# Performance work log

Measured on AMD Instinct MI355X. Metric: run time of the kernel, lower is better.

## Reference

```python
import jax, jax.numpy as jnp
import numpy as np

D_MODEL = 256; N_HEADS = 8; N_LEVELS = 4; N_POINTS = 4
D_HEAD = D_MODEL // N_HEADS


def setup_inputs() -> dict:
    key = jax.random.key(0)
    ks = jax.random.split(key, 8)
    N, Lq = 4, 4096
    shapes = np.array([4096, 2048, 1024, 512], dtype=np.int32)  # temporal lengths per level
    Len_in = int(shapes.sum())  # 7680
    start = np.concatenate([[0], np.cumsum(shapes)[:-1]]).astype(np.int32)
    HLP = N_HEADS * N_LEVELS * N_POINTS
    return {
        "query": jax.random.normal(ks[0], (N, Lq, D_MODEL), jnp.float32),
        "reference_points": jax.random.uniform(ks[1], (N, Lq, N_LEVELS, 1), jnp.float32),
        "input_flatten": jax.random.normal(ks[2], (N, Len_in, D_MODEL), jnp.float32),
        "input_spatial_shapes": jnp.asarray(shapes),
        "input_level_start_index": jnp.asarray(start),
        "W_off": jax.random.normal(ks[3], (D_MODEL, HLP), jnp.float32) * 0.01,
        "b_off": jax.random.normal(ks[4], (HLP,), jnp.float32) * 2.0,
        "W_aw": jax.random.normal(ks[5], (D_MODEL, HLP), jnp.float32) * 0.02,
        "b_aw": jnp.zeros((HLP,), jnp.float32),
        "W_v": jax.random.normal(ks[6], (D_MODEL, D_MODEL), jnp.float32) / np.sqrt(D_MODEL).astype(np.float32),
        "b_v": jnp.zeros((D_MODEL,), jnp.float32),
        "W_out": jax.random.normal(ks[7], (D_MODEL, D_MODEL), jnp.float32) / np.sqrt(D_MODEL).astype(np.float32),
        "b_out": jnp.zeros((D_MODEL,), jnp.float32),
    }


def reference(query, reference_points, input_flatten, input_spatial_shapes,
              input_level_start_index, W_off, b_off, W_aw, b_aw, W_v, b_v,
              W_out, b_out):
    N, Lq, C = query.shape
    M, L, P, Dh = N_HEADS, N_LEVELS, N_POINTS, D_HEAD
    S = input_flatten.shape[1]

    value = (input_flatten @ W_v + b_v).reshape(N, S, M, Dh)
    off = (query @ W_off + b_off).reshape(N, Lq, M, L, P)
    aw = jax.nn.softmax((query @ W_aw + b_aw).reshape(N, Lq, M, L * P), axis=-1)
    aw = aw.reshape(N, Lq, M, L, P)

    # reference_points last dim == 1 branch: loc = ref + off / T_l, in [0,1]
    T = input_spatial_shapes.astype(jnp.float32)[None, None, None, :, None]  # [1,1,1,L,1]
    loc = reference_points[:, :, None, :, None, 0] + off / T  # [N,Lq,M,L,P]

    # grid_sample(align_corners=False, padding_mode='border') along W with H=1, y=0.5:
    # pixel coord x = loc*T - 0.5, clamped to [0, T-1], then linear interp.
    x = jnp.clip(loc * T - 0.5, 0.0, T - 1.0)
    x0 = jnp.floor(x)
    w1 = x - x0                                   # frac weight for right neighbor
    i0 = x0.astype(jnp.int32)
    i1 = jnp.minimum(i0 + 1, input_spatial_shapes[None, None, None, :, None] - 1)
    base = input_level_start_index[None, None, None, :, None]
    g0 = i0 + base                                # global flattened indices [N,Lq,M,L,P]
    g1 = i1 + base

    v = value.transpose(0, 2, 1, 3)               # [N,M,S,Dh]

    def gather(idx):
        idxt = idx.transpose(0, 2, 1, 3, 4).reshape(N, M, Lq * L * P, 1)
        return jnp.take_along_axis(v, idxt, axis=2).reshape(N, M, Lq, L, P, Dh)

    s0 = gather(g0)
    s1 = gather(g1)
    w1t = w1.transpose(0, 2, 1, 3, 4)[..., None]   # [N,M,Lq,L,P,1]
    samp = s0 * (1.0 - w1t) + s1 * w1t             # [N,M,Lq,L,P,Dh]

    awt = aw.transpose(0, 2, 1, 3, 4)[..., None]
    out = (samp * awt).sum(axis=(3, 4))            # [N,M,Lq,Dh]
    out = out.transpose(0, 2, 1, 3).reshape(N, Lq, M * Dh)
    return out @ W_out + b_out
```

## Files before the change

kernel.cpp:

```cpp
#include <hip/hip_runtime.h>
#include <hip/hip_bf16.h>
#include <cstddef>
#include <cstdint>

#define D_MODEL   256
#define N_HEADS   8
#define N_LEVELS  4
#define N_POINTS  4
#define D_HEAD    32
#define HLP       128
#define NBATCH    4
#define LQ        4096
#define S_LEN     7680
#define QB        4

typedef __attribute__((ext_vector_type(8))) short  short8;
typedef __attribute__((ext_vector_type(4))) float  f32x4;
typedef __attribute__((ext_vector_type(8))) unsigned short ushort8;

__device__ __forceinline__ unsigned short f2bf(float x) {
    __hip_bfloat16 h = __float2bfloat16(x);
    return *reinterpret_cast<unsigned short*>(&h);
}
__device__ __forceinline__ float bf2f(unsigned short u) {
    unsigned int v = ((unsigned int)u) << 16;
    return *reinterpret_cast<float*>(&v);
}

__device__ __forceinline__ void gload_lds16(const void* g, void* l) {
    __builtin_amdgcn_global_load_lds(
        (const __attribute__((address_space(1))) void*)g,
        (__attribute__((address_space(3))) void*)l,
        16, 0, 0);
}

__global__ __launch_bounds__(256) void prep_kernel(
    const float* __restrict__ W_v,  const float* __restrict__ W_off,
    const float* __restrict__ W_aw, const float* __restrict__ W_out,
    const float* __restrict__ b_off, const float* __restrict__ b_aw,
    unsigned short* __restrict__ Wv_t, unsigned short* __restrict__ Wcat_t,
    unsigned short* __restrict__ Wout_t, float* __restrict__ bcat)
{
    __shared__ float t[64][65];
    const int z   = blockIdx.z;
    const int k0  = blockIdx.y * 64;
    const int n0  = blockIdx.x * 64;
    const int tid = threadIdx.x;

    const float* src; int srcN; int cs; unsigned short* dst;
    if (z == 0)      { src = W_v;   srcN = 256; cs = n0;       dst = Wv_t;  }
    else if (z == 2) { src = W_out; srcN = 256; cs = n0;       dst = Wout_t;}
    else if (n0 < 128){ src = W_off; srcN = 128; cs = n0;      dst = Wcat_t;}
    else             { src = W_aw;  srcN = 128; cs = n0 - 128; dst = Wcat_t;}

    #pragma unroll
    for (int i = 0; i < 16; ++i) {
        int idx = tid + i * 256;
        int kk = idx >> 6, nn = idx & 63;
        t[kk][nn] = src[(size_t)(k0 + kk) * srcN + cs + nn];
    }
    __syncthreads();
    #pragma unroll
    for (int i = 0; i < 16; ++i) {
        int idx = tid + i * 256;
        int nn = idx >> 6, kk = idx & 63;
        dst[(size_t)(n0 + nn) * 256 + k0 + kk] = f2bf(t[kk][nn]);
    }
    if (z == 1 && blockIdx.x == 0 && blockIdx.y == 0) {
        bcat[tid] = (tid < 128) ? b_off[tid] : b_aw[tid - 128];
    }
}

__global__ __launch_bounds__(256) void gemm_vp_kernel(
    const float* __restrict__ inflat, const float* __restrict__ query,
    const unsigned short* __restrict__ Wv_t, const unsigned short* __restrict__ Wcat_t,
    const float* __restrict__ b_v, const float* __restrict__ bcat,
    unsigned short* __restrict__ value3, float* __restrict__ P)
{
    __shared__ alignas(16) unsigned short Abuf[2][8][64][8];
    __shared__ alignas(16) unsigned short Bbuf[2][8][64][8];

    const int job = blockIdx.x;
    const bool is_val = (job < 480);
    const int jj   = is_val ? job : (job - 480);
    const int row0 = (jj >> 1) * 128;
    const int col0 = (jj & 1) * 128;
    const float* A = is_val ? inflat : query;
    const unsigned short* Bt = is_val ? Wv_t : Wcat_t;
    const float* bias = is_val ? b_v : bcat;

    const int tid  = threadIdx.x;
    const int lane = tid & 63;
    const int w    = tid >> 6;
    const int wm   = w & 1;
    const int wn   = w >> 1;
    const int lr   = lane & 15;
    const int lk   = (lane >> 4) * 8;

    const float* Ap0 = A + (size_t)(row0 + (w * 2 + 0) * 16 + lr) * 256 + lk;
    const float* Ap1 = A + (size_t)(row0 + (w * 2 + 1) * 16 + lr) * 256 + lk;
    const unsigned short* Bcol = Bt + (size_t)(col0 + lr) * 256 + lk;

    f32x4 acc[4][4] = {};

    float4 a00 = *(const float4*)(Ap0), a01 = *(const float4*)(Ap0 + 4);
    float4 a10 = *(const float4*)(Ap1), a11 = *(const float4*)(Ap1 + 4);
    #pragma unroll
    for (int c = 0; c < 2; ++c) {
        const int im = w * 2 + c;
        gload_lds16(Bcol + (size_t)im * 16 * 256, &Bbuf[0][im][0][0]);
    }

    for (int kt = 0; kt < 8; ++kt) {
        const int cur = kt & 1;
        {
            short8 pk;
            pk[0] = (short)f2bf(a00.x); pk[1] = (short)f2bf(a00.y);
            pk[2] = (short)f2bf(a00.z); pk[3] = (short)f2bf(a00.w);
            pk[4] = (short)f2bf(a01.x); pk[5] = (short)f2bf(a01.y);
            pk[6] = (short)f2bf(a01.z); pk[7] = (short)f2bf(a01.w);
            *(short8*)&Abuf[cur][w * 2 + 0][lane][0] = pk;
            pk[0] = (short)f2bf(a10.x); pk[1] = (short)f2bf(a10.y);
            pk[2] = (short)f2bf(a10.z); pk[3] = (short)f2bf(a10.w);
            pk[4] = (short)f2bf(a11.x); pk[5] = (short)f2bf(a11.y);
            pk[6] = (short)f2bf(a11.z); pk[7] = (short)f2bf(a11.w);
            *(short8*)&Abuf[cur][w * 2 + 1][lane][0] = pk;
        }
        __syncthreads();

        if (kt < 7) {
            const int k1 = (kt + 1) * 32;
            a00 = *(const float4*)(Ap0 + k1); a01 = *(const float4*)(Ap0 + k1 + 4);
            a10 = *(const float4*)(Ap1 + k1); a11 = *(const float4*)(Ap1 + k1 + 4);
            #pragma unroll
            for (int c = 0; c < 2; ++c) {
                const int im = w * 2 + c;
                gload_lds16(Bcol + (size_t)im * 16 * 256 + k1, &Bbuf[1 - cur][im][0][0]);
            }
        }

        short8 af[4], bfr[4];
        #pragma unroll
        for (int i = 0; i < 4; ++i) af[i]  = *(const short8*)&Abuf[cur][wm * 4 + i][lane][0];
        #pragma unroll
        for (int j = 0; j < 4; ++j) bfr[j] = *(const short8*)&Bbuf[cur][wn * 4 + j][lane][0];

        #pragma unroll
        for (int i = 0; i < 4; ++i)
            #pragma unroll
            for (int j = 0; j < 4; ++j)
                acc[i][j] = __builtin_amdgcn_mfma_f32_16x16x32_bf16(
                    af[i], bfr[j], acc[i][j], 0, 0, 0);
    }

    const int prow = (lane >> 4) * 4;
    const int pcol = lane & 15;
    if (is_val) {
        const int n  = row0 / S_LEN;
        const int s0 = row0 - n * S_LEN + wm * 64;
        #pragma unroll
        for (int j = 0; j < 4; ++j) {
            const int col = col0 + wn * 64 + j * 16 + pcol;
            const float bs = bias[col];
            const int m = col >> 5, d = col & 31;
            unsigned short* dst = value3 + ((size_t)(n * 8 + m) * S_LEN + s0) * 32 + d;
            #pragma unroll
            for (int i = 0; i < 4; ++i) {
                #pragma unroll
                for (int r = 0; r < 4; ++r) {
                    const int rl = i * 16 + prow + r;
                    dst[(size_t)rl * 32] = f2bf(acc[i][j][r] + bs);
                }
            }
        }
    } else {
        #pragma unroll
        for (int j = 0; j < 4; ++j) {
            const int col = col0 + wn * 64 + j * 16 + pcol;
            const float bs = bias[col];
            #pragma unroll
            for (int i = 0; i < 4; ++i) {
                #pragma unroll
                for (int r = 0; r < 4; ++r) {
                    const int row = row0 + wm * 64 + i * 16 + prow + r;
                    P[(size_t)row * 256 + col] = acc[i][j][r] + bs;
                }
            }
        }
    }
}

__global__ __launch_bounds__(128) void sample_kernel(
    const float* __restrict__ P, const float* __restrict__ refp,
    const int* __restrict__ shapes, const int* __restrict__ lstart,
    const unsigned short* __restrict__ value3,
    unsigned short* __restrict__ tout)
{
    __shared__ int   sG0[QB][130];
    __shared__ float sW [QB][130];
    __shared__ float sA [QB][130];
    __shared__ int   glim[4];

    const int b    = blockIdx.x;
    const int xcd  = b & 7;
    const int n    = xcd >> 1;
    const int half = xcd & 1;
    const int slot = b >> 3;
    const int q0   = (slot * 2 + half) * QB;
    const int nq0  = n * LQ + q0;
    const int tid  = threadIdx.x;

    if (tid < 4) glim[tid] = lstart[tid] + shapes[tid] - 1;

    #pragma unroll
    for (int it = 0; it < 4; ++it) {
        const int idx = tid + it * 128;
        const int q   = idx >> 7;
        const int j   = idx & 127;
        const int l   = (j >> 2) & 3;
        const int nq  = nq0 + q;
        const float off   = __builtin_nontemporal_load(P + (size_t)nq * 256 + j);
        const float logit = __builtin_nontemporal_load(P + (size_t)nq * 256 + 128 + j);
        const float ref   = __builtin_nontemporal_load(refp + (size_t)nq * N_LEVELS + l);
        const int   sh    = shapes[l];
        const float Tf    = (float)sh;
        float x = ref * Tf + off - 0.5f;
        x = fminf(fmaxf(x, 0.0f), Tf - 1.0f);
        const float x0 = floorf(x);
        sG0[q][j] = (int)x0 + lstart[l];
        sW [q][j] = x - x0;
        sA [q][j] = logit;
    }
    __syncthreads();

    const int q  = tid >> 5;
    const int r  = tid & 31;
    const int m  = r >> 2;
    const int ql = r & 3;
    const unsigned short* vb =
        value3 + (size_t)(n * 8 + m) * S_LEN * 32 + ql * 8;

    float e[16];
    float mx = -1e30f;
    #pragma unroll
    for (int i = 0; i < 16; ++i) { e[i] = sA[q][m * 16 + i]; mx = fmaxf(mx, e[i]); }
    float s = 0.f;
    #pragma unroll
    for (int i = 0; i < 16; ++i) { e[i] = __expf(e[i] - mx); s += e[i]; }
    const float rs = 1.0f / s;

    float acc[8] = {};
    #pragma unroll
    for (int c = 0; c < 4; ++c) {
        ushort8 u0[4], u1[4];
        float   aw[4], wl[4];
        #pragma unroll
        for (int i4 = 0; i4 < 4; ++i4) {
            const int i = c * 4 + i4;
            const int j = m * 16 + i;
            aw[i4] = e[i] * rs;
            wl[i4] = sW[q][j];
            const int g0 = sG0[q][j];
            const int g1 = min(g0 + 1, glim[i >> 2]);
            u0[i4] = *(const ushort8*)(vb + (size_t)g0 * 32);
            u1[i4] = *(const ushort8*)(vb + (size_t)g1 * 32);
        }
        #pragma unroll
        for (int i4 = 0; i4 < 4; ++i4) {
            #pragma unroll
            for (int d = 0; d < 8; ++d) {
                const float v0 = bf2f(u0[i4][d]);
                const float v1 = bf2f(u1[i4][d]);
                acc[d] += aw[i4] * (v0 + wl[i4] * (v1 - v0));
            }
        }
    }
    ushort8 o;
    #pragma unroll
    for (int d = 0; d < 8; ++d) o[d] = f2bf(acc[d]);
    __builtin_nontemporal_store(o,
        (ushort8*)(tout + (size_t)(nq0 + q) * 256 + m * 32 + ql * 8));
}

__global__ __launch_bounds__(256) void gemm_out_kernel(
    const unsigned short* __restrict__ A,
    const unsigned short* __restrict__ Bt,
    const float* __restrict__ bias,
    float* __restrict__ Cout)
{
    __shared__ alignas(16) unsigned short Abuf[2][4][64][8];
    __shared__ alignas(16) unsigned short Bbuf[2][8][64][8];

    const int jj   = blockIdx.x;
    const int row0 = (jj >> 1) * 64;
    const int col0 = (jj & 1) * 128;

    const int tid  = threadIdx.x;
    const int lane = tid & 63;
    const int w    = tid >> 6;
    const int wm   = w & 1;
    const int wn   = w >> 1;
    const int lr   = lane & 15;
    const int lk   = (lane >> 4) * 8;

    const unsigned short* Arow = A + (size_t)(row0 + w * 16 + lr) * 256 + lk;
    const unsigned short* Bcol = Bt + (size_t)(col0 + lr) * 256 + lk;

    f32x4 acc[2][4] = {};

    gload_lds16(Arow, &Abuf[0][w][0][0]);
    #pragma unroll
    for (int c = 0; c < 2; ++c) {
        const int im = w * 2 + c;
        gload_lds16(Bcol + (size_t)im * 16 * 256, &Bbuf[0][im][0][0]);
    }

    for (int kt = 0; kt < 8; ++kt) {
        const int cur = kt & 1;
        __syncthreads();

        if (kt < 7) {
            const int k1 = (kt + 1) * 32;
            gload_lds16(Arow + k1, &Abuf[1 - cur][w][0][0]);
            #pragma unroll
            for (int c = 0; c < 2; ++c) {
                const int im = w * 2 + c;
                gload_lds16(Bcol + (size_t)im * 16 * 256 + k1, &Bbuf[1 - cur][im][0][0]);
            }
        }

        short8 af[2], bfr[4];
        #pragma unroll
        for (int i = 0; i < 2; ++i) af[i]  = *(const short8*)&Abuf[cur][wm * 2 + i][lane][0];
        #pragma unroll
        for (int j = 0; j < 4; ++j) bfr[j] = *(const short8*)&Bbuf[cur][wn * 4 + j][lane][0];

        #pragma unroll
        for (int i = 0; i < 2; ++i)
            #pragma unroll
            for (int j = 0; j < 4; ++j)
                acc[i][j] = __builtin_amdgcn_mfma_f32_16x16x32_bf16(
                    af[i], bfr[j], acc[i][j], 0, 0, 0);
    }

    const int prow = (lane >> 4) * 4;
    const int pcol = lane & 15;
    #pragma unroll
    for (int i = 0; i < 2; ++i) {
        #pragma unroll
        for (int j = 0; j < 4; ++j) {
            const int col = col0 + wn * 64 + j * 16 + pcol;
            const float bs = bias[col];
            const int rbase = row0 + wm * 32 + i * 16 + prow;
            #pragma unroll
            for (int r = 0; r < 4; ++r)
                Cout[(size_t)(rbase + r) * 256 + col] = acc[i][j][r] + bs;
        }
    }
}

extern "C" void kernel_launch(void* const* d_in, const int* in_sizes, int n_in,
                              void* d_out, int out_size, void* d_ws, size_t ws_size,
                              hipStream_t stream)
{
    const float* query  = (const float*)d_in[0];
    const float* refp   = (const float*)d_in[1];
    const float* inflat = (const float*)d_in[2];
    const int*   shapes = (const int*)d_in[3];
    const int*   lstart = (const int*)d_in[4];
    const float* W_off  = (const float*)d_in[5];
    const float* b_off  = (const float*)d_in[6];
    const float* W_aw   = (const float*)d_in[7];
    const float* b_aw   = (const float*)d_in[8];
    const float* W_v    = (const float*)d_in[9];
    const float* b_v    = (const float*)d_in[10];
    const float* W_out  = (const float*)d_in[11];
    const float* b_out  = (const float*)d_in[12];

    const int M_val = NBATCH * S_LEN;
    const int M_q   = NBATCH * LQ;

    char* p = (char*)d_ws;
    unsigned short* value3 = (unsigned short*)p; p += (size_t)M_val * D_MODEL * 2;
    float*          P      = (float*)p;          p += (size_t)M_q * 256 * 4;
    unsigned short* tbuf   = (unsigned short*)p; p += (size_t)M_q * D_MODEL * 2;
    unsigned short* Wv_t   = (unsigned short*)p; p += 256 * 256 * 2;
    unsigned short* Wcat_t = (unsigned short*)p; p += 256 * 256 * 2;
    unsigned short* Wout_t = (unsigned short*)p; p += 256 * 256 * 2;
    float*          bcat   = (float*)p;          p += 256 * 4;

    prep_kernel<<<dim3(4, 4, 3), 256, 0, stream>>>(
        W_v, W_off, W_aw, W_out, b_off, b_aw, Wv_t, Wcat_t, Wout_t, bcat);
    gemm_vp_kernel<<<736, 256, 0, stream>>>(
        inflat, query, Wv_t, Wcat_t, b_v, bcat, value3, P);
    sample_kernel<<<4096, 128, 0, stream>>>(
        P, refp, shapes, lstart, value3, tbuf);
    gemm_out_kernel<<<512, 256, 0, stream>>>(
        tbuf, Wout_t, b_out, (float*)d_out);
}
```

Baseline: 168.2 us.

## Pre-convert inputs to bf16, simplify GEMMs, and split sampler across four lanes

Adds a standalone kernel that converts input_flatten and query to bf16 so the projection GEMM can load A tiles directly into LDS. Both GEMMs drop software double-buffering in favour of a simple load-sync-compute-sync loop, and the output GEMM uses larger 128-row tiles. The sampling kernel assigns four threads per output chunk, one per level, and combines them with lane shuffles, using 2 queries per 256-thread block. The extra conversion pass adds global memory traffic, and single buffering exposes load latency in the GEMMs.

New measurement: 177.4 us. 1.05x slower.

```diff
diff --git a/kernel.cpp b/kernel.cpp
--- a/kernel.cpp
+++ b/kernel.cpp
@@ -12,7 +12,7 @@
 #define NBATCH    4
 #define LQ        4096
 #define S_LEN     7680
-#define QB        4
+#define QB        2
 
 typedef __attribute__((ext_vector_type(8))) short  short8;
 typedef __attribute__((ext_vector_type(4))) float  f32x4;
@@ -32,6 +32,24 @@
         (const __attribute__((address_space(1))) void*)g,
         (__attribute__((address_space(3))) void*)l,
         16, 0, 0);
+}
+
+__global__ __launch_bounds__(256) void conv_kernel(
+    const float* __restrict__ inflat, const float* __restrict__ query,
+    unsigned short* __restrict__ inflat_bf, unsigned short* __restrict__ query_bf,
+    int n_val, int n_tot)
+{
+    size_t i = ((size_t)blockIdx.x * blockDim.x + threadIdx.x) * 8;
+    if (i >= (size_t)n_tot) return;
+    const float* src; unsigned short* dst; size_t off;
+    if (i < (size_t)n_val) { src = inflat; dst = inflat_bf; off = i; }
+    else                   { src = query;  dst = query_bf;  off = i - n_val; }
+    float4 a = *(const float4*)(src + off);
+    float4 b = *(const float4*)(src + off + 4);
+    ushort8 r;
+    r[0] = f2bf(a.x); r[1] = f2bf(a.y); r[2] = f2bf(a.z); r[3] = f2bf(a.w);
+    r[4] = f2bf(b.x); r[5] = f2bf(b.y); r[6] = f2bf(b.z); r[7] = f2bf(b.w);
+    *(ushort8*)(dst + off) = r;
 }
 
 __global__ __launch_bounds__(256) void prep_kernel(
@@ -72,20 +90,22 @@
 }
 
 __global__ __launch_bounds__(256) void gemm_vp_kernel(
-    const float* __restrict__ inflat, const float* __restrict__ query,
-    const unsigned short* __restrict__ Wv_t, const unsigned short* __restrict__ Wcat_t,
+    const unsigned short* __restrict__ Abf_val,
+    const unsigned short* __restrict__ Abf_qry,
+    const unsigned short* __restrict__ Wv_t,
+    const unsigned short* __restrict__ Wcat_t,
     const float* __restrict__ b_v, const float* __restrict__ bcat,
     unsigned short* __restrict__ value3, float* __restrict__ P)
 {
-    __shared__ alignas(16) unsigned short Abuf[2][8][64][8];
-    __shared__ alignas(16) unsigned short Bbuf[2][8][64][8];
+    __shared__ alignas(16) unsigned short Als[8][64][8];
+    __shared__ alignas(16) unsigned short Bls[8][64][8];
 
     const int job = blockIdx.x;
     const bool is_val = (job < 480);
     const int jj   = is_val ? job : (job - 480);
     const int row0 = (jj >> 1) * 128;
     const int col0 = (jj & 1) * 128;
-    const float* A = is_val ? inflat : query;
+    const unsigned short* A  = is_val ? Abf_val : Abf_qry;
     const unsigned short* Bt = is_val ? Wv_t : Wcat_t;
     const float* bias = is_val ? b_v : bcat;
 
@@ -97,53 +117,23 @@
     const int lr   = lane & 15;
     const int lk   = (lane >> 4) * 8;
 
-    const float* Ap0 = A + (size_t)(row0 + (w * 2 + 0) * 16 + lr) * 256 + lk;
-    const float* Ap1 = A + (size_t)(row0 + (w * 2 + 1) * 16 + lr) * 256 + lk;
-    const unsigned short* Bcol = Bt + (size_t)(col0 + lr) * 256 + lk;
-
     f32x4 acc[4][4] = {};
 
-    float4 a00 = *(const float4*)(Ap0), a01 = *(const float4*)(Ap0 + 4);
-    float4 a10 = *(const float4*)(Ap1), a11 = *(const float4*)(Ap1 + 4);
-    #pragma unroll
-    for (int c = 0; c < 2; ++c) {
-        const int im = w * 2 + c;
-        gload_lds16(Bcol + (size_t)im * 16 * 256, &Bbuf[0][im][0][0]);
-    }
-
     for (int kt = 0; kt < 8; ++kt) {
-        const int cur = kt & 1;
-        {
-            short8 pk;
-            pk[0] = (short)f2bf(a00.x); pk[1] = (short)f2bf(a00.y);
-            pk[2] = (short)f2bf(a00.z); pk[3] = (short)f2bf(a00.w);
-            pk[4] = (short)f2bf(a01.x); pk[5] = (short)f2bf(a01.y);
-            pk[6] = (short)f2bf(a01.z); pk[7] = (short)f2bf(a01.w);
-            *(short8*)&Abuf[cur][w * 2 + 0][lane][0] = pk;
-            pk[0] = (short)f2bf(a10.x); pk[1] = (short)f2bf(a10.y);
-            pk[2] = (short)f2bf(a10.z); pk[3] = (short)f2bf(a10.w);
-            pk[4] = (short)f2bf(a11.x); pk[5] = (short)f2bf(a11.y);
-            pk[6] = (short)f2bf(a11.z); pk[7] = (short)f2bf(a11.w);
-            *(short8*)&Abuf[cur][w * 2 + 1][lane][0] = pk;
+        const int k0 = kt * 32;
+        #pragma unroll
+        for (int c = 0; c < 2; ++c) {
+            const int im = w * 2 + c;
+            gload_lds16(A  + (size_t)(row0 + im * 16 + lr) * 256 + k0 + lk, &Als[im][0][0]);
+            gload_lds16(Bt + (size_t)(col0 + im * 16 + lr) * 256 + k0 + lk, &Bls[im][0][0]);
         }
         __syncthreads();
 
-        if (kt < 7) {
-            const int k1 = (kt + 1) * 32;
-            a00 = *(const float4*)(Ap0 + k1); a01 = *(const float4*)(Ap0 + k1 + 4);
-            a10 = *(const float4*)(Ap1 + k1); a11 = *(const float4*)(Ap1 + k1 + 4);
-            #pragma unroll
-            for (int c = 0; c < 2; ++c) {
-                const int im = w * 2 + c;
-                gload_lds16(Bcol + (size_t)im * 16 * 256 + k1, &Bbuf[1 - cur][im][0][0]);
-            }
-        }
-
         short8 af[4], bfr[4];
         #pragma unroll
-        for (int i = 0; i < 4; ++i) af[i]  = *(const short8*)&Abuf[cur][wm * 4 + i][lane][0];
-        #pragma unroll
-        for (int j = 0; j < 4; ++j) bfr[j] = *(const short8*)&Bbuf[cur][wn * 4 + j][lane][0];
+        for (int i = 0; i < 4; ++i) af[i]  = *(const short8*)&Als[wm * 4 + i][lane][0];
+        #pragma unroll
+        for (int j = 0; j < 4; ++j) bfr[j] = *(const short8*)&Bls[wn * 4 + j][lane][0];
 
         #pragma unroll
         for (int i = 0; i < 4; ++i)
@@ -151,6 +141,7 @@
             for (int j = 0; j < 4; ++j)
                 acc[i][j] = __builtin_amdgcn_mfma_f32_16x16x32_bf16(
                     af[i], bfr[j], acc[i][j], 0, 0, 0);
+        __syncthreads();
     }
 
     const int prow = (lane >> 4) * 4;
@@ -165,13 +156,10 @@
             const int m = col >> 5, d = col & 31;
             unsigned short* dst = value3 + ((size_t)(n * 8 + m) * S_LEN + s0) * 32 + d;
             #pragma unroll
-            for (int i = 0; i < 4; ++i) {
+            for (int i = 0; i < 4; ++i)
                 #pragma unroll
-                for (int r = 0; r < 4; ++r) {
-                    const int rl = i * 16 + prow + r;
-                    dst[(size_t)rl * 32] = f2bf(acc[i][j][r] + bs);
-                }
-            }
+                for (int r = 0; r < 4; ++r)
+                    dst[(size_t)(i * 16 + prow + r) * 32] = f2bf(acc[i][j][r] + bs);
         }
     } else {
         #pragma unroll
@@ -179,18 +167,79 @@
             const int col = col0 + wn * 64 + j * 16 + pcol;
             const float bs = bias[col];
             #pragma unroll
-            for (int i = 0; i < 4; ++i) {
+            for (int i = 0; i < 4; ++i)
                 #pragma unroll
-                for (int r = 0; r < 4; ++r) {
-                    const int row = row0 + wm * 64 + i * 16 + prow + r;
-                    P[(size_t)row * 256 + col] = acc[i][j][r] + bs;
-                }
-            }
+                for (int r = 0; r < 4; ++r)
+                    P[(size_t)(row0 + wm * 64 + i * 16 + prow + r) * 256 + col]
+                        = acc[i][j][r] + bs;
         }
     }
 }
 
-__global__ __launch_bounds__(128) void sample_kernel(
+__global__ __launch_bounds__(256) void gemm_out_kernel(
+    const unsigned short* __restrict__ A,
+    const unsigned short* __restrict__ Bt,
+    const float* __restrict__ bias,
+    float* __restrict__ Cout)
+{
+    __shared__ alignas(16) unsigned short Als[8][64][8];
+    __shared__ alignas(16) unsigned short Bls[8][64][8];
+
+    const int jj   = blockIdx.x;
+    const int row0 = (jj >> 1) * 128;
+    const int col0 = (jj & 1) * 128;
+
+    const int tid  = threadIdx.x;
+    const int lane = tid & 63;
+    const int w    = tid >> 6;
+    const int wm   = w & 1;
+    const int wn   = w >> 1;
+    const int lr   = lane & 15;
+    const int lk   = (lane >> 4) * 8;
+
+    f32x4 acc[4][4] = {};
+
+    for (int kt = 0; kt < 8; ++kt) {
+        const int k0 = kt * 32;
+        #pragma unroll
+        for (int c = 0; c < 2; ++c) {
+            const int im = w * 2 + c;
+            gload_lds16(A  + (size_t)(row0 + im * 16 + lr) * 256 + k0 + lk, &Als[im][0][0]);
+            gload_lds16(Bt + (size_t)(col0 + im * 16 + lr) * 256 + k0 + lk, &Bls[im][0][0]);
+        }
+        __syncthreads();
+
+        short8 af[4], bfr[4];
+        #pragma unroll
+        for (int i = 0; i < 4; ++i) af[i]  = *(const short8*)&Als[wm * 4 + i][lane][0];
+        #pragma unroll
+        for (int j = 0; j < 4; ++j) bfr[j] = *(const short8*)&Bls[wn * 4 + j][lane][0];
+
+        #pragma unroll
+        for (int i = 0; i < 4; ++i)
+            #pragma unroll
+            for (int j = 0; j < 4; ++j)
+                acc[i][j] = __builtin_amdgcn_mfma_f32_16x16x32_bf16(
+                    af[i], bfr[j], acc[i][j], 0, 0, 0);
+        __syncthreads();
+    }
+
+    const int prow = (lane >> 4) * 4;
+    const int pcol = lane & 15;
+    #pragma unroll
+    for (int j = 0; j < 4; ++j) {
+        const int col = col0 + wn * 64 + j * 16 + pcol;
+        const float bs = bias[col];
+        #pragma unroll
+        for (int i = 0; i < 4; ++i)
+            #pragma unroll
+            for (int r = 0; r < 4; ++r)
+                Cout[(size_t)(row0 + wm * 64 + i * 16 + prow + r) * 256 + col]
+                    = acc[i][j][r] + bs;
+    }
+}
+
+__global__ __launch_bounds__(256) void sample_kernel(
     const float* __restrict__ P, const float* __restrict__ refp,
     const int* __restrict__ shapes, const int* __restrict__ lstart,
     const unsigned short* __restrict__ value3,
@@ -212,13 +261,11 @@
 
     if (tid < 4) glim[tid] = lstart[tid] + shapes[tid] - 1;
 
-    #pragma unroll
-    for (int it = 0; it < 4; ++it) {
-        const int idx = tid + it * 128;
-        const int q   = idx >> 7;
-        const int j   = idx & 127;
-        const int l   = (j >> 2) & 3;
-        const int nq  = nq0 + q;
+    {
+        const int q  = tid >> 7;
+        const int j  = tid & 127;
+        const int l  = (j >> 2) & 3;
+        const int nq = nq0 + q;
         const float off   = __builtin_nontemporal_load(P + (size_t)nq * 256 + j);
         const float logit = __builtin_nontemporal_load(P + (size_t)nq * 256 + 128 + j);
         const float ref   = __builtin_nontemporal_load(refp + (size_t)nq * N_LEVELS + l);
@@ -233,10 +280,10 @@
     }
     __syncthreads();
 
-    const int q  = tid >> 5;
-    const int r  = tid & 31;
-    const int m  = r >> 2;
-    const int ql = r & 3;
+    const int q  = tid >> 7;
+    const int m  = (tid >> 4) & 7;
+    const int ql = (tid >> 2) & 3;
+    const int c  = tid & 3;
     const unsigned short* vb =
         value3 + (size_t)(n * 8 + m) * S_LEN * 32 + ql * 8;
 
@@ -249,113 +296,47 @@
     for (int i = 0; i < 16; ++i) { e[i] = __expf(e[i] - mx); s += e[i]; }
     const float rs = 1.0f / s;
 
+    const int lim = glim[c];
+    ushort8 u0[4], u1[4];
+    float   cw[4];
+    int     g0v[4];
+    #pragma unroll
+    for (int sIdx = 0; sIdx < 4; ++sIdx) {
+        const int j = m * 16 + c * 4 + sIdx;
+        cw[sIdx]  = sW[q][j];
+        g0v[sIdx] = sG0[q][j];
+    }
+    #pragma unroll
+    for (int sIdx = 0; sIdx < 4; ++sIdx) {
+        const int g0 = g0v[sIdx];
+        const int g1 = min(g0 + 1, lim);
+        u0[sIdx] = *(const ushort8*)(vb + (size_t)g0 * 32);
+        u1[sIdx] = *(const ushort8*)(vb + (size_t)g1 * 32);
+    }
+
     float acc[8] = {};
     #pragma unroll
-    for (int c = 0; c < 4; ++c) {
-        ushort8 u0[4], u1[4];
-        float   aw[4], wl[4];
-        #pragma unroll
-        for (int i4 = 0; i4 < 4; ++i4) {
-            const int i = c * 4 + i4;
-            const int j = m * 16 + i;
-            aw[i4] = e[i] * rs;
-            wl[i4] = sW[q][j];
-            const int g0 = sG0[q][j];
-            const int g1 = min(g0 + 1, glim[i >> 2]);
-            u0[i4] = *(const ushort8*)(vb + (size_t)g0 * 32);
-            u1[i4] = *(const ushort8*)(vb + (size_t)g1 * 32);
-        }
-        #pragma unroll
-        for (int i4 = 0; i4 < 4; ++i4) {
-            #pragma unroll
-            for (int d = 0; d < 8; ++d) {
-                const float v0 = bf2f(u0[i4][d]);
-                const float v1 = bf2f(u1[i4][d]);
-                acc[d] += aw[i4] * (v0 + wl[i4] * (v1 - v0));
-            }
-        }
-    }
-    ushort8 o;
-    #pragma unroll
-    for (int d = 0; d < 8; ++d) o[d] = f2bf(acc[d]);
-    __builtin_nontemporal_store(o,
-        (ushort8*)(tout + (size_t)(nq0 + q) * 256 + m * 32 + ql * 8));
-}
-
-__global__ __launch_bounds__(256) void gemm_out_kernel(
-    const unsigned short* __restrict__ A,
-    const unsigned short* __restrict__ Bt,
-    const float* __restrict__ bias,
-    float* __restrict__ Cout)
-{
-    __shared__ alignas(16) unsigned short Abuf[2][4][64][8];
-    __shared__ alignas(16) unsigned short Bbuf[2][8][64][8];
-
-    const int jj   = blockIdx.x;
-    const int row0 = (jj >> 1) * 64;
-    const int col0 = (jj & 1) * 128;
-
-    const int tid  = threadIdx.x;
-    const int lane = tid & 63;
-    const int w    = tid >> 6;
-    const int wm   = w & 1;
-    const int wn   = w >> 1;
-    const int lr   = lane & 15;
-    const int lk   = (lane >> 4) * 8;
-
-    const unsigned short* Arow = A + (size_t)(row0 + w * 16 + lr) * 256 + lk;
-    const unsigned short* Bcol = Bt + (size_t)(col0 + lr) * 256 + lk;
-
-    f32x4 acc[2][4] = {};
-
-    gload_lds16(Arow, &Abuf[0][w][0][0]);
-    #pragma unroll
-    for (int c = 0; c < 2; ++c) {
-        const int im = w * 2 + c;
-        gload_lds16(Bcol + (size_t)im * 16 * 256, &Bbuf[0][im][0][0]);
-    }
-
-    for (int kt = 0; kt < 8; ++kt) {
-        const int cur = kt & 1;
-        __syncthreads();
-
-        if (kt < 7) {
-            const int k1 = (kt + 1) * 32;
-            gload_lds16(Arow + k1, &Abuf[1 - cur][w][0][0]);
-            #pragma unroll
-            for (int c = 0; c < 2; ++c) {
-                const int im = w * 2 + c;
-                gload_lds16(Bcol + (size_t)im * 16 * 256 + k1, &Bbuf[1 - cur][im][0][0]);
-            }
-        }
-
-        short8 af[2], bfr[4];
-        #pragma unroll
-        for (int i = 0; i < 2; ++i) af[i]  = *(const short8*)&Abuf[cur][wm * 2 + i][lane][0];
-        #pragma unroll
-        for (int j = 0; j < 4; ++j) bfr[j] = *(const short8*)&Bbuf[cur][wn * 4 + j][lane][0];
-
-        #pragma unroll
-        for (int i = 0; i < 2; ++i)
-            #pragma unroll
-            for (int j = 0; j < 4; ++j)
-                acc[i][j] = __builtin_amdgcn_mfma_f32_16x16x32_bf16(
-                    af[i], bfr[j], acc[i][j], 0, 0, 0);
-    }
-
-    const int prow = (lane >> 4) * 4;
-    const int pcol = lane & 15;
-    #pragma unroll
-    for (int i = 0; i < 2; ++i) {
-        #pragma unroll
-        for (int j = 0; j < 4; ++j) {
-            const int col = col0 + wn * 64 + j * 16 + pcol;
-            const float bs = bias[col];
-            const int rbase = row0 + wm * 32 + i * 16 + prow;
-            #pragma unroll
-            for (int r = 0; r < 4; ++r)
-                Cout[(size_t)(rbase + r) * 256 + col] = acc[i][j][r] + bs;
-        }
+    for (int sIdx = 0; sIdx < 4; ++sIdx) {
+        const float a  = e[c * 4 + sIdx] * rs;
+        const float w1 = cw[sIdx];
+        const float c0 = a * (1.0f - w1);
+        const float c1 = a * w1;
+        #pragma unroll
+        for (int d = 0; d < 8; ++d)
+            acc[d] += c0 * bf2f(u0[sIdx][d]) + c1 * bf2f(u1[sIdx][d]);
+    }
+
+    #pragma unroll
+    for (int d = 0; d < 8; ++d) {
+        acc[d] += __shfl_xor(acc[d], 1);
+        acc[d] += __shfl_xor(acc[d], 2);
+    }
+    if (c == 0) {
+        ushort8 o;
+        #pragma unroll
+        for (int d = 0; d < 8; ++d) o[d] = f2bf(acc[d]);
+        __builtin_nontemporal_store(o,
+            (ushort8*)(tout + (size_t)(nq0 + q) * 256 + m * 32 + ql * 8));
     }
 }
 
@@ -379,22 +360,29 @@
 
     const int M_val = NBATCH * S_LEN;
     const int M_q   = NBATCH * LQ;
+    const int n_val = M_val * D_MODEL;
+    const int n_q   = M_q * D_MODEL;
+    const int n_tot = n_val + n_q;
 
     char* p = (char*)d_ws;
-    unsigned short* value3 = (unsigned short*)p; p += (size_t)M_val * D_MODEL * 2;
-    float*          P      = (float*)p;          p += (size_t)M_q * 256 * 4;
-    unsigned short* tbuf   = (unsigned short*)p; p += (size_t)M_q * D_MODEL * 2;
-    unsigned short* Wv_t   = (unsigned short*)p; p += 256 * 256 * 2;
-    unsigned short* Wcat_t = (unsigned short*)p; p += 256 * 256 * 2;
-    unsigned short* Wout_t = (unsigned short*)p; p += 256 * 256 * 2;
-    float*          bcat   = (float*)p;          p += 256 * 4;
-
+    unsigned short* value3    = (unsigned short*)p; p += (size_t)n_val * 2;
+    float*          P         = (float*)p;          p += (size_t)M_q * 256 * 4;
+    unsigned short* tbuf      = (unsigned short*)p; p += (size_t)n_q * 2;
+    unsigned short* inflat_bf = (unsigned short*)p; p += (size_t)n_val * 2;
+    unsigned short* query_bf  = (unsigned short*)p; p += (size_t)n_q * 2;
+    unsigned short* Wv_t      = (unsigned short*)p; p += 256 * 256 * 2;
+    unsigned short* Wcat_t    = (unsigned short*)p; p += 256 * 256 * 2;
+    unsigned short* Wout_t    = (unsigned short*)p; p += 256 * 256 * 2;
+    float*          bcat      = (float*)p;          p += 256 * 4;
+
+    conv_kernel<<<(n_tot / 8 + 255) / 256, 256, 0, stream>>>(
+        inflat, query, inflat_bf, query_bf, n_val, n_tot);
     prep_kernel<<<dim3(4, 4, 3), 256, 0, stream>>>(
         W_v, W_off, W_aw, W_out, b_off, b_aw, Wv_t, Wcat_t, Wout_t, bcat);
     gemm_vp_kernel<<<736, 256, 0, stream>>>(
-        inflat, query, Wv_t, Wcat_t, b_v, bcat, value3, P);
-    sample_kernel<<<4096, 128, 0, stream>>>(
+        inflat_bf, query_bf, Wv_t, Wcat_t, b_v, bcat, value3, P);
+    sample_kernel<<<8192, 256, 0, stream>>>(
         P, refp, shapes, lstart, value3, tbuf);
-    gemm_out_kernel<<<512, 256, 0, stream>>>(
+    gemm_out_kernel<<<256, 256, 0, stream>>>(
         tbuf, Wout_t, b_out, (float*)d_out);
 }
```
